# Kernel optimization log

Hardware: AMD Instinct MI355X
Metric: run time of the kernel (lower is better)

Reference implementation:

```python
import jax, jax.numpy as jnp
import numpy as np

# Offsets from TransformerStateEncoder (external constants, fixed here)
START, END = 0, 128
D_MODEL = 256
NUM_BET_BINS = 16
LN_EPS = 1e-5


def setup_inputs() -> dict:
    key = jax.random.key(0)
    ks = jax.random.split(key, 10)
    B, S = 2048, 160
    # token_ids < 0 marks invalid slots (~1/6 of positions)
    token_ids = jax.random.randint(ks[0], (B, S), -1, 5, dtype=jnp.int32)
    action_actors = jax.random.randint(ks[1], (B, S), 0, 2, dtype=jnp.int32)
    action_streets = jax.random.randint(ks[2], (B, S), 0, 4, dtype=jnp.int32)
    action_legal_masks = (jax.random.uniform(ks[3], (B, S, NUM_BET_BINS)) < 0.5).astype(jnp.float32)
    # Learned parameters
    actor_w = jax.random.normal(ks[4], (2, D_MODEL), dtype=jnp.float32) * 0.02
    street_w = jax.random.normal(ks[5], (4, D_MODEL), dtype=jnp.float32) * 0.02
    pos_w = jax.random.normal(ks[6], (END - START, D_MODEL), dtype=jnp.float32) * 0.02
    mlp_w = jax.random.normal(ks[7], (NUM_BET_BINS, D_MODEL), dtype=jnp.float32) * (1.0 / np.sqrt(NUM_BET_BINS))
    mlp_b = jnp.zeros((D_MODEL,), jnp.float32)
    ln_g = jnp.ones((D_MODEL,), jnp.float32)
    ln_b = jnp.zeros((D_MODEL,), jnp.float32)
    return dict(token_ids=token_ids, action_actors=action_actors,
                action_streets=action_streets, action_legal_masks=action_legal_masks,
                actor_w=actor_w, street_w=street_w, pos_w=pos_w,
                mlp_w=mlp_w, mlp_b=mlp_b, ln_g=ln_g, ln_b=ln_b)


def reference(token_ids, action_actors, action_streets, action_legal_masks,
              actor_w, street_w, pos_w, mlp_w, mlp_b, ln_g, ln_b):
    # Slice the action-token window
    actors = action_actors[:, START:END]            # [B, L]
    streets = action_streets[:, START:END]          # [B, L]
    masks = action_legal_masks[:, START:END, :].astype(jnp.float32)  # [B, L, K]
    valid = (token_ids[:, START:END] >= 0)[..., None]               # [B, L, 1]

    # Legal-mask MLP: Linear -> LayerNorm -> ReLU (Dropout is identity in eval)
    h = jnp.einsum('blk,kd->bld', masks, mlp_w) + mlp_b
    mu = jnp.mean(h, axis=-1, keepdims=True)
    var = jnp.mean(jnp.square(h - mu), axis=-1, keepdims=True)
    hn = (h - mu) * jax.lax.rsqrt(var + LN_EPS) * ln_g + ln_b
    legal_emb = jax.nn.relu(hn)                     # [B, L, D]

    pos_emb = pos_w[None, :, :]                     # positions 0..L-1, [1, L, D]
    combined = actor_w[actors] + street_w[streets] + pos_emb + legal_emb

    # Scatter-back semantics: zeros at invalid slots
    return jnp.where(valid, combined, jnp.zeros((), combined.dtype))
```

## Files before the change

### kernel.cpp

```cpp
#include <hip/hip_runtime.h>

#define BATCH   2048
#define SEQ     160
#define LOUT    128
#define D_MODEL 256
#define NBINS   16
#define LN_EPS  1e-5f

typedef float f32x4 __attribute__((ext_vector_type(4)));

#define T0_OFF  0
#define T1_OFF  65536
#define P_OFF   131072
#define WS_FLOATS (P_OFF + 1024 * D_MODEL)

__global__ __launch_bounds__(256)
void build_tables_kernel(const float* __restrict__ actor_w,
                         const float* __restrict__ street_w,
                         const float* __restrict__ pos_w,
                         const float* __restrict__ mlp_w,
                         const float* __restrict__ mlp_b,
                         float* __restrict__ ws)
{
    const int bid = blockIdx.x;
    const int d   = threadIdx.x;
    if (bid < 256) {
        const int c = bid;
        float s = mlp_b[d];
#pragma unroll
        for (int k = 0; k < 8; ++k)
            s = fmaf((float)((c >> k) & 1), mlp_w[k * D_MODEL + d], s);
        ws[T0_OFF + c * D_MODEL + d] = s;
    } else if (bid < 512) {
        const int c = bid - 256;
        float s = 0.0f;
#pragma unroll
        for (int k = 0; k < 8; ++k)
            s = fmaf((float)((c >> k) & 1), mlp_w[(8 + k) * D_MODEL + d], s);
        ws[T1_OFF + c * D_MODEL + d] = s;
    } else {
        const int i  = bid - 512;
        const int a  = i >> 9;
        const int st = (i >> 7) & 3;
        const int l  = i & 127;
        ws[P_OFF + i * D_MODEL + d] =
            actor_w[a * D_MODEL + d] + street_w[st * D_MODEL + d] + pos_w[l * D_MODEL + d];
    }
}

__global__ __launch_bounds__(256)
void action_embedding_kernel(const int*   __restrict__ token_ids,
                             const int*   __restrict__ action_actors,
                             const int*   __restrict__ action_streets,
                             const float* __restrict__ legal_masks,
                             const float* __restrict__ ln_g,
                             const float* __restrict__ ln_b,
                             const float* __restrict__ ws,
                             float*       __restrict__ out)
{
    const int lane = threadIdx.x & 63;
    const int wave = threadIdx.x >> 6;
    const int d0   = lane << 2;

    const float4 g4  = *reinterpret_cast<const float4*>(&ln_g[d0]);
    const float4 lb4 = *reinterpret_cast<const float4*>(&ln_b[d0]);

    const float* T0 = ws + T0_OFF;
    const float* T1 = ws + T1_OFF;
    const float* P  = ws + P_OFF;

    const int total = BATCH * LOUT;
    const int wid   = blockIdx.x * 4 + wave;
    const int nw    = gridDim.x * 4;

    for (int idx = wid; idx < total; idx += nw) {
        const int b = idx >> 7;
        const int l = idx & 127;
        const int off = __builtin_amdgcn_readfirstlane(b * SEQ + l);

        const int tok = token_ids[off];
        const int a   = action_actors[off];
        const int st  = action_streets[off];

        const unsigned* mw = reinterpret_cast<const unsigned*>(&legal_masks[(size_t)off * NBINS]);
        unsigned c0 = 0u, c1 = 0u;
#pragma unroll
        for (int k = 0; k < 8; ++k) {
            c0 |= (mw[k]     ? 1u : 0u) << k;
            c1 |= (mw[k + 8] ? 1u : 0u) << k;
        }
        const int i0 = __builtin_amdgcn_readfirstlane((int)c0);
        const int i1 = __builtin_amdgcn_readfirstlane((int)c1);

        const float4 t0 = *reinterpret_cast<const float4*>(&T0[i0 * D_MODEL + d0]);
        const float4 t1 = *reinterpret_cast<const float4*>(&T1[i1 * D_MODEL + d0]);
        float4 h;
        h.x = t0.x + t1.x;  h.y = t0.y + t1.y;
        h.z = t0.z + t1.z;  h.w = t0.w + t1.w;

        float s  = h.x + h.y + h.z + h.w;
        float ss = fmaf(h.x, h.x, fmaf(h.y, h.y, fmaf(h.z, h.z, h.w * h.w)));
#pragma unroll
        for (int o = 32; o > 0; o >>= 1) {
            s  += __shfl_xor(s,  o);
            ss += __shfl_xor(ss, o);
        }
        const float mu   = s * (1.0f / D_MODEL);
        const float var  = ss * (1.0f / D_MODEL) - mu * mu;
        const float rstd = rsqrtf(var + LN_EPS);

        const int pidx = __builtin_amdgcn_readfirstlane((((a << 2) | st) << 7) | l);
        const float4 pw = *reinterpret_cast<const float4*>(&P[(size_t)pidx * D_MODEL + d0]);

        const float vfl = (tok >= 0) ? 1.0f : 0.0f;

        f32x4 o;
        o.x = (fmaxf((h.x - mu) * rstd * g4.x + lb4.x, 0.0f) + pw.x) * vfl;
        o.y = (fmaxf((h.y - mu) * rstd * g4.y + lb4.y, 0.0f) + pw.y) * vfl;
        o.z = (fmaxf((h.z - mu) * rstd * g4.z + lb4.z, 0.0f) + pw.z) * vfl;
        o.w = (fmaxf((h.w - mu) * rstd * g4.w + lb4.w, 0.0f) + pw.w) * vfl;

        __builtin_nontemporal_store(o, reinterpret_cast<f32x4*>(&out[(size_t)idx * D_MODEL + d0]));
    }
}

extern "C" void kernel_launch(void* const* d_in, const int* in_sizes, int n_in,
                              void* d_out, int out_size, void* d_ws, size_t ws_size,
                              hipStream_t stream) {
    const int*   token_ids      = (const int*)  d_in[0];
    const int*   action_actors  = (const int*)  d_in[1];
    const int*   action_streets = (const int*)  d_in[2];
    const float* legal_masks    = (const float*)d_in[3];
    const float* actor_w        = (const float*)d_in[4];
    const float* street_w       = (const float*)d_in[5];
    const float* pos_w          = (const float*)d_in[6];
    const float* mlp_w          = (const float*)d_in[7];
    const float* mlp_b          = (const float*)d_in[8];
    const float* ln_g           = (const float*)d_in[9];
    const float* ln_b           = (const float*)d_in[10];
    float* out = (float*)d_out;
    float* ws  = (float*)d_ws;

    hipLaunchKernelGGL(build_tables_kernel, dim3(1536), dim3(256), 0, stream,
                       actor_w, street_w, pos_w, mlp_w, mlp_b, ws);

    hipLaunchKernelGGL(action_embedding_kernel, dim3(2048), dim3(256), 0, stream,
                       token_ids, action_actors, action_streets, legal_masks,
                       ln_g, ln_b, ws, out);
}
```

Measured before the change: 376.3 us.

## Precompute LayerNorm stats per mask combo and process two rows per wave

Adds a kernel that precomputes mean and mean-square of the MLP output for every pair of 8-bit mask codes, so the main kernel looks up LayerNorm statistics instead of doing cross-lane shuffle reductions. Mask bits are now gathered with one coalesced load and a ballot instead of 16 scalar loads, and each wave handles two output rows per iteration to increase memory-level parallelism. This costs an extra kernel launch and a 65536-entry stats table in workspace.

```diff
diff --git a/kernel.cpp b/kernel.cpp
--- a/kernel.cpp
+++ b/kernel.cpp
@@ -12,7 +12,9 @@
 #define T0_OFF  0
 #define T1_OFF  65536
 #define P_OFF   131072
-#define WS_FLOATS (P_OFF + 1024 * D_MODEL)
+#define MU_OFF  393216
+#define Q_OFF   458752
+#define WS_FLOATS 524288
 
 __global__ __launch_bounds__(256)
 void build_tables_kernel(const float* __restrict__ actor_w,
@@ -49,6 +51,27 @@
 }
 
 __global__ __launch_bounds__(256)
+void build_stats_kernel(float* __restrict__ ws)
+{
+    const int c0 = blockIdx.x;
+    const int c1 = threadIdx.x;
+    const float* r0 = ws + T0_OFF + c0 * D_MODEL;
+    const float* r1 = ws + T1_OFF + c1 * D_MODEL;
+    float sm = 0.0f, sq = 0.0f;
+#pragma unroll 8
+    for (int d4 = 0; d4 < D_MODEL / 4; ++d4) {
+        const float4 a = *reinterpret_cast<const float4*>(&r0[d4 * 4]);
+        const float4 b = *reinterpret_cast<const float4*>(&r1[d4 * 4]);
+        const float hx = a.x + b.x, hy = a.y + b.y, hz = a.z + b.z, hw = a.w + b.w;
+        sm += hx + hy + hz + hw;
+        sq = fmaf(hx, hx, fmaf(hy, hy, fmaf(hz, hz, fmaf(hw, hw, sq))));
+    }
+    const int idx = (c0 << 8) | c1;
+    ws[MU_OFF + idx] = sm * (1.0f / D_MODEL);
+    ws[Q_OFF  + idx] = sq * (1.0f / D_MODEL);
+}
+
+__global__ __launch_bounds__(256, 6)
 void action_embedding_kernel(const int*   __restrict__ token_ids,
                              const int*   __restrict__ action_actors,
                              const int*   __restrict__ action_streets,
@@ -68,59 +91,71 @@
     const float* T0 = ws + T0_OFF;
     const float* T1 = ws + T1_OFF;
     const float* P  = ws + P_OFF;
+    const float* MU = ws + MU_OFF;
+    const float* Q  = ws + Q_OFF;
 
-    const int total = BATCH * LOUT;
-    const int wid   = blockIdx.x * 4 + wave;
-    const int nw    = gridDim.x * 4;
+    const int mrow = (lane >> 4) & 1;
+    const int melt = lane & 15;
 
-    for (int idx = wid; idx < total; idx += nw) {
-        const int b = idx >> 7;
-        const int l = idx & 127;
-        const int off = __builtin_amdgcn_readfirstlane(b * SEQ + l);
+    const int npairs = (BATCH * LOUT) / 2;
+    const int wid    = blockIdx.x * 4 + wave;
+    const int nw     = gridDim.x * 4;
 
-        const int tok = token_ids[off];
-        const int a   = action_actors[off];
-        const int st  = action_streets[off];
+    for (int c = wid; c < npairs; c += nw) {
+        const int rowA = c * 2;
+        const int b    = rowA >> 7;
+        const int l0   = rowA & 127;
+        const int off  = __builtin_amdgcn_readfirstlane(b * SEQ + l0);
 
-        const unsigned* mw = reinterpret_cast<const unsigned*>(&legal_masks[(size_t)off * NBINS]);
-        unsigned c0 = 0u, c1 = 0u;
-#pragma unroll
-        for (int k = 0; k < 8; ++k) {
-            c0 |= (mw[k]     ? 1u : 0u) << k;
-            c1 |= (mw[k + 8] ? 1u : 0u) << k;
+        const float mv = legal_masks[(size_t)off * NBINS + mrow * NBINS + melt];
+        const unsigned long long bm = __ballot(mv != 0.0f);
+        const unsigned lo  = (unsigned)bm;
+        const int i0a = lo & 0xFF,          i1a = (lo >> 8)  & 0xFF;
+        const int i0b = (lo >> 16) & 0xFF,  i1b = (lo >> 24) & 0xFF;
+
+        const int tokA = token_ids[off],      tokB = token_ids[off + 1];
+        const int aA   = action_actors[off],  aB   = action_actors[off + 1];
+        const int stA  = action_streets[off], stB  = action_streets[off + 1];
+
+        const float muA = MU[(i0a << 8) | i1a];
+        const float qA  = Q [(i0a << 8) | i1a];
+        const float muB = MU[(i0b << 8) | i1b];
+        const float qB  = Q [(i0b << 8) | i1b];
+        const float rstdA = rsqrtf(qA - muA * muA + LN_EPS);
+        const float rstdB = rsqrtf(qB - muB * muB + LN_EPS);
+
+        const float4 t0a = *reinterpret_cast<const float4*>(&T0[i0a * D_MODEL + d0]);
+        const float4 t1a = *reinterpret_cast<const float4*>(&T1[i1a * D_MODEL + d0]);
+        const float4 t0b = *reinterpret_cast<const float4*>(&T0[i0b * D_MODEL + d0]);
+        const float4 t1b = *reinterpret_cast<const float4*>(&T1[i1b * D_MODEL + d0]);
+        const int pidxA = (((aA << 2) | stA) << 7) | l0;
+        const int pidxB = (((aB << 2) | stB) << 7) | (l0 + 1);
+        const float4 pwa = *reinterpret_cast<const float4*>(&P[(size_t)pidxA * D_MODEL + d0]);
+        const float4 pwb = *reinterpret_cast<const float4*>(&P[(size_t)pidxB * D_MODEL + d0]);
+
+        const float vA = (tokA >= 0) ? 1.0f : 0.0f;
+        const float vB = (tokB >= 0) ? 1.0f : 0.0f;
+
+        f32x4 oA, oB;
+        {
+            const float hx = t0a.x + t1a.x, hy = t0a.y + t1a.y,
+                        hz = t0a.z + t1a.z, hw = t0a.w + t1a.w;
+            oA.x = (fmaxf((hx - muA) * rstdA * g4.x + lb4.x, 0.0f) + pwa.x) * vA;
+            oA.y = (fmaxf((hy - muA) * rstdA * g4.y + lb4.y, 0.0f) + pwa.y) * vA;
+            oA.z = (fmaxf((hz - muA) * rstdA * g4.z + lb4.z, 0.0f) + pwa.z) * vA;
+            oA.w = (fmaxf((hw - muA) * rstdA * g4.w + lb4.w, 0.0f) + pwa.w) * vA;
         }
-        const int i0 = __builtin_amdgcn_readfirstlane((int)c0);
-        const int i1 = __builtin_amdgcn_readfirstlane((int)c1);
+        {
+            const float hx = t0b.x + t1b.x, hy = t0b.y + t1b.y,
+                        hz = t0b.z + t1b.z, hw = t0b.w + t1b.w;
+            oB.x = (fmaxf((hx - muB) * rstdB * g4.x + lb4.x, 0.0f) + pwb.x) * vB;
+            oB.y = (fmaxf((hy - muB) * rstdB * g4.y + lb4.y, 0.0f) + pwb.y) * vB;
+            oB.z = (fmaxf((hz - muB) * rstdB * g4.z + lb4.z, 0.0f) + pwb.z) * vB;
+            oB.w = (fmaxf((hw - muB) * rstdB * g4.w + lb4.w, 0.0f) + pwb.w) * vB;
+        }
 
-        const float4 t0 = *reinterpret_cast<const float4*>(&T0[i0 * D_MODEL + d0]);
-        const float4 t1 = *reinterpret_cast<const float4*>(&T1[i1 * D_MODEL + d0]);
-        float4 h;
-        h.x = t0.x + t1.x;  h.y = t0.y + t1.y;
-        h.z = t0.z + t1.z;  h.w = t0.w + t1.w;
-
-        float s  = h.x + h.y + h.z + h.w;
-        float ss = fmaf(h.x, h.x, fmaf(h.y, h.y, fmaf(h.z, h.z, h.w * h.w)));
-#pragma unroll
-        for (int o = 32; o > 0; o >>= 1) {
-            s  += __shfl_xor(s,  o);
-            ss += __shfl_xor(ss, o);
-        }
-        const float mu   = s * (1.0f / D_MODEL);
-        const float var  = ss * (1.0f / D_MODEL) - mu * mu;
-        const float rstd = rsqrtf(var + LN_EPS);
-
-        const int pidx = __builtin_amdgcn_readfirstlane((((a << 2) | st) << 7) | l);
-        const float4 pw = *reinterpret_cast<const float4*>(&P[(size_t)pidx * D_MODEL + d0]);
-
-        const float vfl = (tok >= 0) ? 1.0f : 0.0f;
-
-        f32x4 o;
-        o.x = (fmaxf((h.x - mu) * rstd * g4.x + lb4.x, 0.0f) + pw.x) * vfl;
-        o.y = (fmaxf((h.y - mu) * rstd * g4.y + lb4.y, 0.0f) + pw.y) * vfl;
-        o.z = (fmaxf((h.z - mu) * rstd * g4.z + lb4.z, 0.0f) + pw.z) * vfl;
-        o.w = (fmaxf((h.w - mu) * rstd * g4.w + lb4.w, 0.0f) + pw.w) * vfl;
-
-        __builtin_nontemporal_store(o, reinterpret_cast<f32x4*>(&out[(size_t)idx * D_MODEL + d0]));
+        __builtin_nontemporal_store(oA, reinterpret_cast<f32x4*>(&out[(size_t)rowA * D_MODEL + d0]));
+        __builtin_nontemporal_store(oB, reinterpret_cast<f32x4*>(&out[((size_t)rowA + 1) * D_MODEL + d0]));
     }
 }
 
@@ -143,7 +178,7 @@
 
     hipLaunchKernelGGL(build_tables_kernel, dim3(1536), dim3(256), 0, stream,
                        actor_w, street_w, pos_w, mlp_w, mlp_b, ws);
-
+    hipLaunchKernelGGL(build_stats_kernel, dim3(256), dim3(256), 0, stream, ws);
     hipLaunchKernelGGL(action_embedding_kernel, dim3(2048), dim3(256), 0, stream,
                        token_ids, action_actors, action_streets, legal_masks,
                        ln_g, ln_b, ws, out);
```

Measured after the change: 362.2 us. 3.7% less time.
